# Optimization experiments

Hardware: AMD Instinct MI355X
Metric: run time of the kernel (lower is better)

Reference implementation:

```python
import jax, jax.numpy as jnp
import numpy as np

B, T, H, C = 128, 1024, 512, 10


def setup_inputs() -> dict:
    key = jax.random.key(0)
    ks = jax.random.split(key, 8)
    s = 1.0 / np.sqrt(H)  # PyTorch LSTMCell/Linear default init scale
    return {
        "x": jax.random.normal(ks[0], (B, T), jnp.float32),
        "w_ih": jax.random.uniform(ks[1], (4 * H, 1), jnp.float32, -s, s),
        "w_hh": jax.random.uniform(ks[2], (4 * H, H), jnp.float32, -s, s),
        "b_ih": jax.random.uniform(ks[3], (4 * H,), jnp.float32, -s, s),
        "b_hh": jax.random.uniform(ks[4], (4 * H,), jnp.float32, -s, s),
        "w_t": jax.random.normal(ks[5], (2 * H, 1), jnp.float32) * 0.02,
        "w_fc": jax.random.uniform(ks[6], (C, H), jnp.float32, -s, s),
        "b_fc": jax.random.uniform(ks[7], (C,), jnp.float32, -s, s),
    }


def reference(x, w_ih, w_hh, b_ih, b_hh, w_t, w_fc, b_fc):
    # x: [B, T] scalar-per-step sequence (input_size == 1 in the original)
    Bz = x.shape[0]
    Hh = w_hh.shape[1]
    w1 = w_t[:Hh, 0]   # multiplies the new hidden h_t       [H]
    w2 = w_t[Hh:, 0]   # multiplies each history state h_j   [H]
    bias = b_ih + b_hh
    wih_row = w_ih[:, 0]  # [4H], since input_size == 1

    # Original computes, at step i, attn_c = sum_{j<=i} ((h_new@w1 + h_j@w2) * h_j)
    # over history [h_init=0, h_1, ..., h_i]. We keep running sums:
    #   S1 = sum_j h_j,   S2 = sum_j (h_j@w2) * h_j
    # so attn_c = (h_new@w1) * S1 + S2  -- identical math, O(T) instead of O(T^2).
    def step(carry, x_t):
        h, c, S1, S2 = carry
        gates = x_t[:, None] * wih_row[None, :] + h @ w_hh.T + bias  # [B,4H]
        i_g, f_g, g_g, o_g = jnp.split(gates, 4, axis=1)  # PyTorch gate order i,f,g,o
        c_new = jax.nn.sigmoid(f_g) * c + jax.nn.sigmoid(i_g) * jnp.tanh(g_g)
        h_new = jax.nn.sigmoid(o_g) * jnp.tanh(c_new)
        a = (h_new @ w1)[:, None]          # [B,1]
        attn = a * S1 + S2                 # [B,H]
        S1 = S1 + h_new
        S2 = S2 + (h_new @ w2)[:, None] * h_new
        return (h_new, c_new, S1, S2), (h_new, attn)

    z = jnp.zeros((Bz, Hh), x.dtype)
    _, (hs, attns) = jax.lax.scan(step, (z, z, z, z), x.T)  # [T,B,H] each
    out = jnp.transpose(hs + attns, (1, 0, 2))               # [B,T,H]
    return out @ w_fc.T + b_fc                               # [B,T,C]
```

## Files before the change

### kernel.cpp

```cpp
#include <hip/hip_runtime.h>
#include <math.h>

typedef __attribute__((ext_vector_type(8))) short bf16x8;
typedef __attribute__((ext_vector_type(4))) float f32x4;

static constexpr int Tt = 1024;
static constexpr int Hh = 512;
static constexpr int Cc = 10;

static constexpr int NXCD = 8;
static constexpr int BPX  = 32;
static constexpr int UPB  = 16;
static constexpr int NB   = 16;
static constexpr int THREADS = 512;
static constexpr int GRID = 256;

static constexpr size_t WS_HHI_B = 4096;
static constexpr size_t WS_HLO_B = 4096 + 262144;

__device__ __forceinline__ unsigned short f2bf(float f) {
    unsigned u = __builtin_bit_cast(unsigned, f);
    return (unsigned short)((u + 0x7FFFu + ((u >> 16) & 1u)) >> 16);
}
__device__ __forceinline__ float bf2f(unsigned short h) {
    unsigned u = ((unsigned)h) << 16;
    return __builtin_bit_cast(float, u);
}
__device__ __forceinline__ float dot4(float4 a, float4 b) {
    return a.x * b.x + a.y * b.y + a.z * b.z + a.w * b.w;
}
__device__ __forceinline__ float fsig(float x) {
    const float e = __builtin_amdgcn_exp2f(x * -1.44269504f);
    return __builtin_amdgcn_rcpf(1.0f + e);
}
__device__ __forceinline__ float ftanh(float x) {
    const float e = __builtin_amdgcn_exp2f(x * -2.88539008f);
    return 2.0f * __builtin_amdgcn_rcpf(1.0f + e) - 1.0f;
}

__global__ __launch_bounds__(THREADS, 2)
void lstm_fused(const float* __restrict__ x,
                const float* __restrict__ w_ih,
                const float* __restrict__ w_hh,
                const float* __restrict__ b_ih,
                const float* __restrict__ b_hh,
                const float* __restrict__ w_t,
                const float* __restrict__ w_fc,
                const float* __restrict__ b_fc,
                float* __restrict__ out,
                float* __restrict__ ws)
{
    const int tid   = threadIdx.x;
    const int lane  = tid & 63;
    const int wv    = tid >> 6;
    const int mpair = wv & 1;
    const int kq    = wv >> 1;
    const int frow  = lane & 15;
    const int kgrp  = lane >> 4;

    int* flags    = (int*)ws;
    int* counters = (int*)ws + 256;
    unsigned short* hg_hi = (unsigned short*)((char*)ws + WS_HHI_B);
    unsigned short* hg_lo = (unsigned short*)((char*)ws + WS_HLO_B);

    __shared__ __align__(16) short hhi_ls[2][16 * 512];
    __shared__ __align__(16) short hlo_ls[2][16 * 512];
    __shared__ __align__(16) float gbuf[4 * 64 * 20];
    int* xchg = (int*)gbuf;

    if (tid == 0) {
        int xr;
        asm volatile("s_getreg_b32 %0, hwreg(20, 0, 32)" : "=s"(xr));
        const int xcd = xr & 7;
        xchg[0] = xcd;
        xchg[1] = atomicAdd(&counters[xcd * 32], 1) & 31;
    }
    __syncthreads();
    const int xcd  = xchg[0];
    const int rank = xchg[1];
    __syncthreads();
    const int fbase = xcd * BPX;

    bf16x8 wahi[2][4], walo[2][4];
    #pragma unroll
    for (int mt = 0; mt < 2; ++mt) {
        const int gate = mpair * 2 + mt;
        const float* wr = w_hh + (size_t)(gate * Hh + rank * UPB + frow) * Hh;
        #pragma unroll
        for (int kk = 0; kk < 4; ++kk) {
            const float4* s = (const float4*)(wr + (kq * 4 + kk) * 32 + kgrp * 8);
            const float4 f0 = s[0], f1 = s[1];
            const float f[8] = { f0.x, f0.y, f0.z, f0.w, f1.x, f1.y, f1.z, f1.w };
            bf16x8 vhi, vlo;
            #pragma unroll
            for (int j = 0; j < 8; ++j) {
                const unsigned short hb = f2bf(f[j]);
                vhi[j] = (short)hb;
                vlo[j] = (short)f2bf(f[j] - bf2f(hb));
            }
            wahi[mt][kk] = vhi;
            walo[mt][kk] = vlo;
        }
    }

    const int u  = tid & 15;
    const int b_ = (tid >> 4) & 15;
    const int gj = rank * UPB + u;
    const int gb = xcd * NB + b_;
    float wih_r[4], bias_r[4];
    #pragma unroll
    for (int g = 0; g < 4; ++g) {
        wih_r[g]  = w_ih[g * Hh + gj];
        bias_r[g] = b_ih[g * Hh + gj] + b_hh[g * Hh + gj];
    }
    float creg = 0.0f;

    const bool owner = (rank < NB);
    const int  gb_own = xcd * NB + rank;
    float S1w[Cc], S2w[Cc], bfc_r[Cc];
    #pragma unroll
    for (int c = 0; c < Cc; ++c) { S1w[c] = 0.f; S2w[c] = 0.f; bfc_r[c] = b_fc[c]; }

    for (int t = 0; t <= Tt; ++t) {
        const int rb = t & 1, wb = rb ^ 1;
        char* Lhi = (char*)hhi_ls[rb];
        char* Llo = (char*)hlo_ls[rb];

        if (t == 0) {
            const bf16x8 z = { 0, 0, 0, 0, 0, 0, 0, 0 };
            #pragma unroll
            for (int it = 0; it < 2; ++it) {
                const int idx = it * 512 + tid;
                const int row = idx >> 6, kg = idx & 63;
                const int off = (row * 1024 + kg * 16) ^ ((row & 7) << 4);
                *(bf16x8*)(Lhi + off) = z;
                *(bf16x8*)(Llo + off) = z;
            }
        } else if (t < Tt) {
            const bf16x8* shi = (const bf16x8*)(hg_hi + (size_t)(rb * NXCD + xcd) * NB * Hh);
            const bf16x8* slo = (const bf16x8*)(hg_lo + (size_t)(rb * NXCD + xcd) * NB * Hh);
            #pragma unroll
            for (int it = 0; it < 2; ++it) {
                const int idx = it * 512 + tid;
                const int row = idx >> 6, kg = idx & 63;
                const bf16x8 vhi = shi[idx];
                const bf16x8 vlo = slo[idx];
                const int off = (row * 1024 + kg * 16) ^ ((row & 7) << 4);
                *(bf16x8*)(Lhi + off) = vhi;
                *(bf16x8*)(Llo + off) = vlo;
            }
        }

        if (t > 0 && wv == 0 && owner) {
            const size_t rbase = ((size_t)(rb * NXCD + xcd) * NB + rank) * Hh + lane * 8;
            const bf16x8 vh = *(const bf16x8*)(hg_hi + rbase);
            const bf16x8 vl = *(const bf16x8*)(hg_lo + rbase);
            float f[8];
            #pragma unroll
            for (int j = 0; j < 8; ++j)
                f[j] = bf2f((unsigned short)vh[j]) + bf2f((unsigned short)vl[j]);
            const float4 hA = make_float4(f[0], f[1], f[2], f[3]);
            const float4 hB = make_float4(f[4], f[5], f[6], f[7]);
            const float4* wt4 = (const float4*)w_t;
            const float4* wf4 = (const float4*)w_fc;
            float r[12];
            r[0] = dot4(hA, wt4[lane * 2])       + dot4(hB, wt4[lane * 2 + 1]);
            r[1] = dot4(hA, wt4[128 + lane * 2]) + dot4(hB, wt4[128 + lane * 2 + 1]);
            #pragma unroll
            for (int c = 0; c < Cc; ++c)
                r[2 + c] = dot4(hA, wf4[c * 128 + lane * 2])
                         + dot4(hB, wf4[c * 128 + lane * 2 + 1]);
            #pragma unroll
            for (int m = 1; m <= 32; m <<= 1)
                #pragma unroll
                for (int k2 = 0; k2 < 12; ++k2)
                    r[k2] += __shfl_xor(r[k2], m, 64);

            if (lane == 0) {
                const float a = r[0], b2 = r[1];
                float* po = out + ((size_t)gb_own * Tt + (t - 1)) * Cc;
                #pragma unroll
                for (int c = 0; c < Cc; ++c) {
                    const float hw = r[2 + c];
                    po[c] = hw + a * S1w[c] + S2w[c] + bfc_r[c];
                    S1w[c] += hw;
                    S2w[c] += b2 * hw;
                }
            }
        }
        if (t == Tt) break;

        float xv = 0.f;
        if (tid < 256) xv = x[(size_t)gb * Tt + t];
        __syncthreads();

        f32x4 acc[2][3];
        #pragma unroll
        for (int mt = 0; mt < 2; ++mt)
            #pragma unroll
            for (int p = 0; p < 3; ++p)
                acc[mt][p] = f32x4{ 0.f, 0.f, 0.f, 0.f };

        #pragma unroll
        for (int kk = 0; kk < 4; ++kk) {
            const int kabs = kq * 4 + kk;
            const int bo = (frow * 1024 + kgrp * 16 + kabs * 64) ^ ((lane & 7) << 4);
            const bf16x8 bhi = *(const bf16x8*)(Lhi + bo);
            const bf16x8 blo = *(const bf16x8*)(Llo + bo);
            #pragma unroll
            for (int mt = 0; mt < 2; ++mt) {
                acc[mt][0] = __builtin_amdgcn_mfma_f32_16x16x32_bf16(wahi[mt][kk], bhi, acc[mt][0], 0, 0, 0);
                acc[mt][1] = __builtin_amdgcn_mfma_f32_16x16x32_bf16(wahi[mt][kk], blo, acc[mt][1], 0, 0, 0);
                acc[mt][2] = __builtin_amdgcn_mfma_f32_16x16x32_bf16(walo[mt][kk], bhi, acc[mt][2], 0, 0, 0);
            }
        }
        {
            const int u0 = kgrp * 4;
            #pragma unroll
            for (int mt = 0; mt < 2; ++mt) {
                const int g = mpair * 2 + mt;
                #pragma unroll
                for (int r = 0; r < 4; ++r)
                    gbuf[(kq * 64 + g * 16 + u0 + r) * 20 + frow] =
                        acc[mt][0][r] + acc[mt][1][r] + acc[mt][2][r];
            }
        }
        __syncthreads();

        if (tid < 256) {
            float gs[4];
            #pragma unroll
            for (int g = 0; g < 4; ++g) {
                const int base = (g * 16 + u) * 20 + b_;
                gs[g] = gbuf[base] + gbuf[base + 1280]
                      + gbuf[base + 2560] + gbuf[base + 3840];
            }
            const float gi = gs[0] + xv * wih_r[0] + bias_r[0];
            const float gf = gs[1] + xv * wih_r[1] + bias_r[1];
            const float gg = gs[2] + xv * wih_r[2] + bias_r[2];
            const float go = gs[3] + xv * wih_r[3] + bias_r[3];
            creg = fsig(gf) * creg + fsig(gi) * ftanh(gg);
            const float hnew = fsig(go) * ftanh(creg);
            const unsigned short hb2 = f2bf(hnew);
            const unsigned short lb2 = f2bf(hnew - bf2f(hb2));
            const size_t hoff = ((size_t)(wb * NXCD + xcd) * NB + b_) * Hh + gj;
            hg_hi[hoff] = hb2;
            hg_lo[hoff] = lb2;
        }
        __syncthreads();

        if (tid == 0)
            *(volatile int*)(flags + fbase + rank) = t + 1;

        if (tid < 32) {
            const volatile int* fl = (const volatile int*)(flags + fbase + tid);
            int v = *fl;
            while (__any(v < t + 1)) {
                __builtin_amdgcn_s_sleep(1);
                asm volatile("buffer_inv\n\ts_waitcnt vmcnt(0)" ::: "memory");
                v = *fl;
            }
            asm volatile("buffer_inv\n\ts_waitcnt vmcnt(0)" ::: "memory");
        }
        __syncthreads();
    }
}

extern "C" void kernel_launch(void* const* d_in, const int* in_sizes, int n_in,
                              void* d_out, int out_size, void* d_ws, size_t ws_size,
                              hipStream_t stream)
{
    const float* xp  = (const float*)d_in[0];
    const float* wih = (const float*)d_in[1];
    const float* whh = (const float*)d_in[2];
    const float* bih = (const float*)d_in[3];
    const float* bhh = (const float*)d_in[4];
    const float* wt  = (const float*)d_in[5];
    const float* wfc = (const float*)d_in[6];
    const float* bfc = (const float*)d_in[7];
    float* outp = (float*)d_out;
    float* ws   = (float*)d_ws;

    (void)hipMemsetAsync(d_ws, 0, 4096, stream);

    hipLaunchKernelGGL(lstm_fused, dim3(GRID), dim3(THREADS), 0, stream,
                       xp, wih, whh, bih, bhh, wt, wfc, bfc, outp, ws);
}
```

Before: 5.254 ms.

## Read hidden state directly from global into MFMA, split gates per wave

Drops the per-step LDS staging of the hidden state: each of four compute waves now owns one gate over the full K=512 and loads B fragments straight from global memory, which removes the 4-way K-split reduction and one barrier. A fifth wave takes over the output projection, so it runs alongside the matvec instead of before it. Block size falls to 320 threads, and a large padding array keeps LDS usage high, apparently to hold occupancy where it was. The trade-off is more global/L2 load latency on the critical path each step and more weight registers per wave (16 fragment pairs).

Result: slower. 13.05 ms (+148.4%).

```diff
diff --git a/kernel.cpp b/kernel.cpp
--- a/kernel.cpp
+++ b/kernel.cpp
@@ -12,7 +12,7 @@
 static constexpr int BPX  = 32;
 static constexpr int UPB  = 16;
 static constexpr int NB   = 16;
-static constexpr int THREADS = 512;
+static constexpr int THREADS = 320;
 static constexpr int GRID = 256;
 
 static constexpr size_t WS_HHI_B = 4096;
@@ -50,23 +50,20 @@
                 float* __restrict__ out,
                 float* __restrict__ ws)
 {
-    const int tid   = threadIdx.x;
-    const int lane  = tid & 63;
-    const int wv    = tid >> 6;
-    const int mpair = wv & 1;
-    const int kq    = wv >> 1;
-    const int frow  = lane & 15;
-    const int kgrp  = lane >> 4;
+    const int tid  = threadIdx.x;
+    const int lane = tid & 63;
+    const int wv   = tid >> 6;
+    const int frow = lane & 15;
+    const int kgrp = lane >> 4;
 
     int* flags    = (int*)ws;
     int* counters = (int*)ws + 256;
     unsigned short* hg_hi = (unsigned short*)((char*)ws + WS_HHI_B);
     unsigned short* hg_lo = (unsigned short*)((char*)ws + WS_HLO_B);
 
-    __shared__ __align__(16) short hhi_ls[2][16 * 512];
-    __shared__ __align__(16) short hlo_ls[2][16 * 512];
-    __shared__ __align__(16) float gbuf[4 * 64 * 20];
-    int* xchg = (int*)gbuf;
+    __shared__ __align__(16) float gbuf[64 * 20];
+    __shared__ int lds_pad[20480];
+    int* xchg = lds_pad;
 
     if (tid == 0) {
         int xr;
@@ -81,14 +78,12 @@
     __syncthreads();
     const int fbase = xcd * BPX;
 
-    bf16x8 wahi[2][4], walo[2][4];
-    #pragma unroll
-    for (int mt = 0; mt < 2; ++mt) {
-        const int gate = mpair * 2 + mt;
-        const float* wr = w_hh + (size_t)(gate * Hh + rank * UPB + frow) * Hh;
+    bf16x8 wahi[16], walo[16];
+    if (wv < 4) {
+        const float* wr = w_hh + (size_t)(wv * Hh + rank * UPB + frow) * Hh;
         #pragma unroll
-        for (int kk = 0; kk < 4; ++kk) {
-            const float4* s = (const float4*)(wr + (kq * 4 + kk) * 32 + kgrp * 8);
+        for (int kk = 0; kk < 16; ++kk) {
+            const float4* s = (const float4*)(wr + kk * 32 + kgrp * 8);
             const float4 f0 = s[0], f1 = s[1];
             const float f[8] = { f0.x, f0.y, f0.z, f0.w, f1.x, f1.y, f1.z, f1.w };
             bf16x8 vhi, vlo;
@@ -98,8 +93,8 @@
                 vhi[j] = (short)hb;
                 vlo[j] = (short)f2bf(f[j] - bf2f(hb));
             }
-            wahi[mt][kk] = vhi;
-            walo[mt][kk] = vlo;
+            wahi[kk] = vhi;
+            walo[kk] = vlo;
         }
     }
 
@@ -123,69 +118,67 @@
 
     for (int t = 0; t <= Tt; ++t) {
         const int rb = t & 1, wb = rb ^ 1;
-        char* Lhi = (char*)hhi_ls[rb];
-        char* Llo = (char*)hlo_ls[rb];
-
-        if (t == 0) {
-            const bf16x8 z = { 0, 0, 0, 0, 0, 0, 0, 0 };
-            #pragma unroll
-            for (int it = 0; it < 2; ++it) {
-                const int idx = it * 512 + tid;
-                const int row = idx >> 6, kg = idx & 63;
-                const int off = (row * 1024 + kg * 16) ^ ((row & 7) << 4);
-                *(bf16x8*)(Lhi + off) = z;
-                *(bf16x8*)(Llo + off) = z;
-            }
-        } else if (t < Tt) {
-            const bf16x8* shi = (const bf16x8*)(hg_hi + (size_t)(rb * NXCD + xcd) * NB * Hh);
-            const bf16x8* slo = (const bf16x8*)(hg_lo + (size_t)(rb * NXCD + xcd) * NB * Hh);
-            #pragma unroll
-            for (int it = 0; it < 2; ++it) {
-                const int idx = it * 512 + tid;
-                const int row = idx >> 6, kg = idx & 63;
-                const bf16x8 vhi = shi[idx];
-                const bf16x8 vlo = slo[idx];
-                const int off = (row * 1024 + kg * 16) ^ ((row & 7) << 4);
-                *(bf16x8*)(Lhi + off) = vhi;
-                *(bf16x8*)(Llo + off) = vlo;
-            }
-        }
-
-        if (t > 0 && wv == 0 && owner) {
-            const size_t rbase = ((size_t)(rb * NXCD + xcd) * NB + rank) * Hh + lane * 8;
-            const bf16x8 vh = *(const bf16x8*)(hg_hi + rbase);
-            const bf16x8 vl = *(const bf16x8*)(hg_lo + rbase);
-            float f[8];
-            #pragma unroll
-            for (int j = 0; j < 8; ++j)
-                f[j] = bf2f((unsigned short)vh[j]) + bf2f((unsigned short)vl[j]);
-            const float4 hA = make_float4(f[0], f[1], f[2], f[3]);
-            const float4 hB = make_float4(f[4], f[5], f[6], f[7]);
-            const float4* wt4 = (const float4*)w_t;
-            const float4* wf4 = (const float4*)w_fc;
-            float r[12];
-            r[0] = dot4(hA, wt4[lane * 2])       + dot4(hB, wt4[lane * 2 + 1]);
-            r[1] = dot4(hA, wt4[128 + lane * 2]) + dot4(hB, wt4[128 + lane * 2 + 1]);
-            #pragma unroll
-            for (int c = 0; c < Cc; ++c)
-                r[2 + c] = dot4(hA, wf4[c * 128 + lane * 2])
-                         + dot4(hB, wf4[c * 128 + lane * 2 + 1]);
-            #pragma unroll
-            for (int m = 1; m <= 32; m <<= 1)
-                #pragma unroll
-                for (int k2 = 0; k2 < 12; ++k2)
-                    r[k2] += __shfl_xor(r[k2], m, 64);
-
-            if (lane == 0) {
-                const float a = r[0], b2 = r[1];
-                float* po = out + ((size_t)gb_own * Tt + (t - 1)) * Cc;
-                #pragma unroll
-                for (int c = 0; c < Cc; ++c) {
-                    const float hw = r[2 + c];
-                    po[c] = hw + a * S1w[c] + S2w[c] + bfc_r[c];
-                    S1w[c] += hw;
-                    S2w[c] += b2 * hw;
+        const unsigned short* hbase_hi = hg_hi + (size_t)(rb * NXCD + xcd) * NB * Hh;
+        const unsigned short* hbase_lo = hg_lo + (size_t)(rb * NXCD + xcd) * NB * Hh;
+
+        if (wv == 4) {
+            if (t > 0 && owner) {
+                const size_t rbase = (size_t)rank * Hh + lane * 8;
+                const bf16x8 vh = *(const bf16x8*)(hbase_hi + rbase);
+                const bf16x8 vl = *(const bf16x8*)(hbase_lo + rbase);
+                float f[8];
+                #pragma unroll
+                for (int j = 0; j < 8; ++j)
+                    f[j] = bf2f((unsigned short)vh[j]) + bf2f((unsigned short)vl[j]);
+                const float4 hA = make_float4(f[0], f[1], f[2], f[3]);
+                const float4 hB = make_float4(f[4], f[5], f[6], f[7]);
+                const float4* wt4 = (const float4*)w_t;
+                const float4* wf4 = (const float4*)w_fc;
+                float r[12];
+                r[0] = dot4(hA, wt4[lane * 2])       + dot4(hB, wt4[lane * 2 + 1]);
+                r[1] = dot4(hA, wt4[128 + lane * 2]) + dot4(hB, wt4[128 + lane * 2 + 1]);
+                #pragma unroll
+                for (int c = 0; c < Cc; ++c)
+                    r[2 + c] = dot4(hA, wf4[c * 128 + lane * 2])
+                             + dot4(hB, wf4[c * 128 + lane * 2 + 1]);
+                #pragma unroll
+                for (int m = 1; m <= 32; m <<= 1)
+                    #pragma unroll
+                    for (int k2 = 0; k2 < 12; ++k2)
+                        r[k2] += __shfl_xor(r[k2], m, 64);
+
+                if (lane == 0) {
+                    const float a = r[0], b2 = r[1];
+                    float* po = out + ((size_t)gb_own * Tt + (t - 1)) * Cc;
+                    #pragma unroll
+                    for (int c = 0; c < Cc; ++c) {
+                        const float hw = r[2 + c];
+                        po[c] = hw + a * S1w[c] + S2w[c] + bfc_r[c];
+                        S1w[c] += hw;
+                        S2w[c] += b2 * hw;
+                    }
                 }
+            }
+        } else {
+            f32x4 a0 = { 0.f, 0.f, 0.f, 0.f };
+            f32x4 a1 = { 0.f, 0.f, 0.f, 0.f };
+            f32x4 a2 = { 0.f, 0.f, 0.f, 0.f };
+            if (t > 0 && t < Tt) {
+                const unsigned short* ph = hbase_hi + (size_t)frow * Hh + kgrp * 8;
+                const unsigned short* pl = hbase_lo + (size_t)frow * Hh + kgrp * 8;
+                #pragma unroll 4
+                for (int kk = 0; kk < 16; ++kk) {
+                    const bf16x8 bhi = *(const bf16x8*)(ph + kk * 32);
+                    const bf16x8 blo = *(const bf16x8*)(pl + kk * 32);
+                    a0 = __builtin_amdgcn_mfma_f32_16x16x32_bf16(wahi[kk], bhi, a0, 0, 0, 0);
+                    a1 = __builtin_amdgcn_mfma_f32_16x16x32_bf16(wahi[kk], blo, a1, 0, 0, 0);
+                    a2 = __builtin_amdgcn_mfma_f32_16x16x32_bf16(walo[kk], bhi, a2, 0, 0, 0);
+                }
+            }
+            if (t < Tt) {
+                #pragma unroll
+                for (int r = 0; r < 4; ++r)
+                    gbuf[(wv * 16 + kgrp * 4 + r) * 20 + frow] = a0[r] + a1[r] + a2[r];
             }
         }
         if (t == Tt) break;
@@ -194,51 +187,11 @@
         if (tid < 256) xv = x[(size_t)gb * Tt + t];
         __syncthreads();
 
-        f32x4 acc[2][3];
-        #pragma unroll
-        for (int mt = 0; mt < 2; ++mt)
-            #pragma unroll
-            for (int p = 0; p < 3; ++p)
-                acc[mt][p] = f32x4{ 0.f, 0.f, 0.f, 0.f };
-
-        #pragma unroll
-        for (int kk = 0; kk < 4; ++kk) {
-            const int kabs = kq * 4 + kk;
-            const int bo = (frow * 1024 + kgrp * 16 + kabs * 64) ^ ((lane & 7) << 4);
-            const bf16x8 bhi = *(const bf16x8*)(Lhi + bo);
-            const bf16x8 blo = *(const bf16x8*)(Llo + bo);
-            #pragma unroll
-            for (int mt = 0; mt < 2; ++mt) {
-                acc[mt][0] = __builtin_amdgcn_mfma_f32_16x16x32_bf16(wahi[mt][kk], bhi, acc[mt][0], 0, 0, 0);
-                acc[mt][1] = __builtin_amdgcn_mfma_f32_16x16x32_bf16(wahi[mt][kk], blo, acc[mt][1], 0, 0, 0);
-                acc[mt][2] = __builtin_amdgcn_mfma_f32_16x16x32_bf16(walo[mt][kk], bhi, acc[mt][2], 0, 0, 0);
-            }
-        }
-        {
-            const int u0 = kgrp * 4;
-            #pragma unroll
-            for (int mt = 0; mt < 2; ++mt) {
-                const int g = mpair * 2 + mt;
-                #pragma unroll
-                for (int r = 0; r < 4; ++r)
-                    gbuf[(kq * 64 + g * 16 + u0 + r) * 20 + frow] =
-                        acc[mt][0][r] + acc[mt][1][r] + acc[mt][2][r];
-            }
-        }
-        __syncthreads();
-
         if (tid < 256) {
-            float gs[4];
-            #pragma unroll
-            for (int g = 0; g < 4; ++g) {
-                const int base = (g * 16 + u) * 20 + b_;
-                gs[g] = gbuf[base] + gbuf[base + 1280]
-                      + gbuf[base + 2560] + gbuf[base + 3840];
-            }
-            const float gi = gs[0] + xv * wih_r[0] + bias_r[0];
-            const float gf = gs[1] + xv * wih_r[1] + bias_r[1];
-            const float gg = gs[2] + xv * wih_r[2] + bias_r[2];
-            const float go = gs[3] + xv * wih_r[3] + bias_r[3];
+            const float gi = gbuf[(0 * 16 + u) * 20 + b_] + xv * wih_r[0] + bias_r[0];
+            const float gf = gbuf[(1 * 16 + u) * 20 + b_] + xv * wih_r[1] + bias_r[1];
+            const float gg = gbuf[(2 * 16 + u) * 20 + b_] + xv * wih_r[2] + bias_r[2];
+            const float go = gbuf[(3 * 16 + u) * 20 + b_] + xv * wih_r[3] + bias_r[3];
             creg = fsig(gf) * creg + fsig(gi) * ftanh(gg);
             const float hnew = fsig(go) * ftanh(creg);
             const unsigned short hb2 = f2bf(hnew);
```
